# Kernel tuning notes

Hardware: AMD Instinct MI355X
Metric: run time of the kernel (lower is better)

The kernel has to match this reference:

```python
import jax, jax.numpy as jnp
import numpy as np

DEPTH = 256
HEADS = 8
K = 128          # kernel_size == attended axis length (height)
DH = DEPTH // HEADS  # 32
EPS = 1e-5


def _bn(x, gamma, beta, axes):
    # training-mode batch norm (biased variance), per-channel on axis 1
    mean = jnp.mean(x, axis=axes, keepdims=True)
    var = jnp.var(x, axis=axes, keepdims=True)
    shape = [1] * x.ndim
    shape[1] = x.shape[1]
    g = gamma.reshape(shape)
    b = beta.reshape(shape)
    return (x - mean) * jax.lax.rsqrt(var + EPS) * g + b


def setup_inputs() -> dict:
    key = jax.random.key(0)
    ks = jax.random.split(key, 3)
    x = jax.random.normal(ks[0], (2, DEPTH, K, K), dtype=jnp.float32)
    w_kqv = jax.random.normal(ks[1], (2 * DEPTH, DEPTH), dtype=jnp.float32) * 0.05
    rel_encoding = jax.random.normal(ks[2], (2 * DH, 2 * K - 1), dtype=jnp.float32)
    return {
        "x": x,
        "w_kqv": w_kqv,
        "kqv_gamma": jnp.ones((2 * DEPTH,), jnp.float32),
        "kqv_beta": jnp.zeros((2 * DEPTH,), jnp.float32),
        "logits_gamma": jnp.ones((3 * HEADS,), jnp.float32),
        "logits_beta": jnp.zeros((3 * HEADS,), jnp.float32),
        "rel_encoding": rel_encoding,
    }


def reference(x, w_kqv, kqv_gamma, kqv_beta, logits_gamma, logits_beta, rel_encoding):
    B, C, H, W = x.shape  # height_dim=True path
    # (B,C,H,W) -> (B,W,C,H) -> (B*W, C, H)
    xf = jnp.transpose(x, (0, 3, 1, 2)).reshape(B * W, C, H)
    # 1x1 conv == channel matmul
    kqv = jnp.einsum('oc,bch->boh', w_kqv, xf)  # (BW, 2*depth, H)
    kqv = _bn(kqv, kqv_gamma, kqv_beta, axes=(0, 2))
    kqv = kqv.reshape(B * W, HEADS, 2 * DH, H)
    k = kqv[:, :, : DH // 2]            # (BW, h, dh/2, H)
    q = kqv[:, :, DH // 2: DH]          # (BW, h, dh/2, H)
    v = kqv[:, :, DH:]                  # (BW, h, dh,   H)

    # relative position gather: (2*dh, 2K-1) -> (2*dh, K, K)
    idx = (jnp.arange(K)[None, :] - jnp.arange(K)[:, None] + K - 1).reshape(-1)
    rel = rel_encoding[:, idx].reshape(2 * DH, K, K)
    q_enc = rel[: DH // 2]
    k_enc = rel[DH // 2: DH]
    v_enc = rel[DH:]

    qk = jnp.einsum('bhdx,bhdy->bhxy', q, k)
    qr = jnp.einsum('bhdx,dxy->bhxy', q, q_enc)
    kr = jnp.swapaxes(jnp.einsum('bhdx,dxy->bhxy', k, k_enc), 2, 3)
    logits = jnp.concatenate([qk, qr, kr], axis=1)  # (BW, 3*h, K, K)
    logits = _bn(logits, logits_gamma, logits_beta, axes=(0, 2, 3))
    logits = logits.reshape(B * W, 3, HEADS, H, H).sum(axis=1)
    weights = jax.nn.softmax(logits, axis=3)  # (BW, h, K, K)

    attn = jnp.einsum('bhxy,bhdy->bhdx', weights, v)         # (BW, h, dh, H)
    attn_enc = jnp.einsum('bhxy,dxy->bhdx', weights, v_enc)  # (BW, h, dh, H)
    out = (attn + attn_enc).reshape(B, W, DEPTH, H)  # cat+reshape+sum(dim=-2) == add
    out = jnp.transpose(out, (0, 2, 3, 1))  # (B, depth, H, W)
    return out
```

## Files before the change

### kernel.cpp

```cpp
#include <hip/hip_runtime.h>
#include <hip/hip_bf16.h>

#define H 128
#define NB 256
#define OC 512
#define CIN 256
#define NN 16384
#define EPS 1e-5f

#define EQG_OFF 524288
#define EKG_OFF 589824
#define EVG_OFF 655360

typedef __attribute__((ext_vector_type(4))) float f32x4;
typedef __attribute__((ext_vector_type(8))) short bf16x8;
typedef unsigned short u16x8 __attribute__((ext_vector_type(8)));

__device__ __forceinline__ float bf2f(unsigned short u){
    return __uint_as_float(((unsigned int)u) << 16);
}
__device__ __forceinline__ unsigned short f2bf(float f){
    unsigned int r;
    asm("v_cvt_pk_bf16_f32 %0, %1, %2" : "=v"(r) : "v"(f), "v"(f));
    return (unsigned short)r;
}
__device__ __forceinline__ float ldin(const void* p, size_t i, bool f32){
    return f32 ? ((const float*)p)[i] : bf2f(((const unsigned short*)p)[i]);
}
__device__ __forceinline__ short ld_bf16(const void* p, size_t i, bool f32){
    if (f32) return (short)f2bf(((const float*)p)[i]);
    return ((const short*)p)[i];
}
__device__ __forceinline__ bool probe_f32(const void* gamma_ones){
    return *(const unsigned int*)gamma_ones == 0x3F800000u;
}

template<bool F32>
__device__ __forceinline__ void gemm_body(const void* __restrict__ w,
                                          const void* __restrict__ x,
                                          unsigned short* __restrict__ c1,
                                          short (*As)[128][40], short (*Bs)[64][40])
{
    const int m0 = blockIdx.x * 128;
    const int n0 = blockIdx.y * 64;
    const int b0 = blockIdx.z;
    const int t  = threadIdx.x;
    const int lane = t & 63, wv = t >> 6;
    const int wm = wv & 1, wn = wv >> 1;
    const int lm = lane & 15, quad = lane >> 4;
    const size_t xb = (size_t)b0 * CIN * NN;
    const int am = t >> 1, ak = (t & 1) * 16;
    const int bn = t & 63, bk = (t >> 6) * 8;

    float4 pa[4]; float pb[8];
    u16x8 qa[2]; unsigned short qb[8];

    auto load_tile = [&](int k0){
        if constexpr (F32){
            const float* wp = (const float*)w + (size_t)(m0+am)*CIN + k0 + ak;
            #pragma unroll
            for (int q=0;q<4;q++) pa[q] = *(const float4*)(wp + 4*q);
            const float* xp = (const float*)x + xb + (size_t)(k0+bk)*NN + n0 + bn;
            #pragma unroll
            for (int i=0;i<8;i++) pb[i] = xp[(size_t)i*NN];
        } else {
            const unsigned short* wp = (const unsigned short*)w + (size_t)(m0+am)*CIN + k0 + ak;
            qa[0] = *(const u16x8*)wp; qa[1] = *(const u16x8*)(wp+8);
            const unsigned short* xp = (const unsigned short*)x + xb + (size_t)(k0+bk)*NN + n0 + bn;
            #pragma unroll
            for (int i=0;i<8;i++) qb[i] = xp[(size_t)i*NN];
        }
    };
    auto store_tile = [&](int buf){
        if constexpr (F32){
            short ta[16];
            #pragma unroll
            for (int q=0;q<4;q++){
                ta[4*q+0]=(short)f2bf(pa[q].x); ta[4*q+1]=(short)f2bf(pa[q].y);
                ta[4*q+2]=(short)f2bf(pa[q].z); ta[4*q+3]=(short)f2bf(pa[q].w);
            }
            *(bf16x8*)&As[buf][am][ak]   = *(bf16x8*)&ta[0];
            *(bf16x8*)&As[buf][am][ak+8] = *(bf16x8*)&ta[8];
            #pragma unroll
            for (int i=0;i<8;i++) Bs[buf][bn][bk+i] = (short)f2bf(pb[i]);
        } else {
            *(u16x8*)&As[buf][am][ak]   = qa[0];
            *(u16x8*)&As[buf][am][ak+8] = qa[1];
            #pragma unroll
            for (int i=0;i<8;i++) Bs[buf][bn][bk+i] = (short)qb[i];
        }
    };

    f32x4 acc[4][2];
    #pragma unroll
    for (int i=0;i<4;i++){ acc[i][0]=(f32x4){0,0,0,0}; acc[i][1]=(f32x4){0,0,0,0}; }

    load_tile(0); store_tile(0); __syncthreads();
    for (int kk=0; kk<8; ++kk){
        const int cur = kk & 1;
        if (kk < 7) load_tile((kk+1)*32);
        bf16x8 af[4], bfB[2];
        #pragma unroll
        for (int i=0;i<4;i++) af[i]  = *(const bf16x8*)&As[cur][wm*64 + i*16 + lm][quad*8];
        #pragma unroll
        for (int j=0;j<2;j++) bfB[j] = *(const bf16x8*)&Bs[cur][wn*32 + j*16 + lm][quad*8];
        #pragma unroll
        for (int i=0;i<4;i++)
            #pragma unroll
            for (int j=0;j<2;j++)
                acc[i][j] = __builtin_amdgcn_mfma_f32_16x16x32_bf16(af[i], bfB[j], acc[i][j], 0,0,0);
        if (kk < 7) store_tile(cur ^ 1);
        __syncthreads();
    }
    #pragma unroll
    for (int i=0;i<4;i++){
        #pragma unroll
        for (int j=0;j<2;j++){
            int n = n0 + wn*32 + j*16 + lm;
            #pragma unroll
            for (int r=0;r<4;r++){
                int m = m0 + wm*64 + i*16 + quad*4 + r;
                c1[((size_t)b0*OC + m)*NN + n] = f2bf(acc[i][j][r]);
            }
        }
    }
}

__global__ __launch_bounds__(256) void k_gemm(const void* __restrict__ w,
                                              const void* __restrict__ x,
                                              unsigned short* __restrict__ c1,
                                              const void* __restrict__ probe)
{
    __shared__ short As[2][128][40];
    __shared__ short Bs[2][64][40];
    if (probe_f32(probe)) gemm_body<true >(w, x, c1, As, Bs);
    else                  gemm_body<false>(w, x, c1, As, Bs);
}

__global__ __launch_bounds__(256) void k_bn_transpose(const unsigned short* __restrict__ c1,
        unsigned short* __restrict__ kqvt,
        const void* __restrict__ gamma, const void* __restrict__ beta)
{
    __shared__ short T[128][130];
    __shared__ float red[8];
    __shared__ float sc_sh[2];
    const bool f32 = probe_f32(gamma);
    const int o = blockIdx.x;
    const int t = threadIdx.x;
    const int lane = t & 63, wv = t >> 6;
    const u16x8* r08 = (const u16x8*)(c1 + (size_t)o*NN);
    const u16x8* r18 = (const u16x8*)(c1 + ((size_t)OC + o)*NN);
    float s=0.f, ss=0.f;
    #pragma unroll
    for (int i=0;i<8;i++){
        u16x8 a = r08[t + i*256];
        u16x8 b = r18[t + i*256];
        #pragma unroll
        for (int e=0;e<8;e++){
            float va = bf2f(a[e]); s += va; ss = fmaf(va,va,ss);
            float vb = bf2f(b[e]); s += vb; ss = fmaf(vb,vb,ss);
        }
    }
    #pragma unroll
    for (int off=1; off<64; off<<=1){ s += __shfl_xor(s,off); ss += __shfl_xor(ss,off); }
    if (lane==0){ red[wv*2] = s; red[wv*2+1] = ss; }
    __syncthreads();
    if (t==0){
        float st=0.f, sq=0.f;
        for (int i=0;i<4;i++){ st += red[i*2]; sq += red[i*2+1]; }
        float mean = st * (1.f/32768.f);
        float var  = sq * (1.f/32768.f) - mean*mean;
        float scale = ldin(gamma, o, f32) * rsqrtf(var + EPS);
        sc_sh[0] = scale;
        sc_sh[1] = ldin(beta, o, f32) - mean*scale;
    }
    __syncthreads();
    const float scale = sc_sh[0], shift = sc_sh[1];
    for (int b0=0;b0<2;b0++){
        const u16x8* r8 = b0 ? r18 : r08;
        #pragma unroll
        for (int i=0;i<8;i++){
            int vi = t + i*256;
            u16x8 a = r8[vi];
            int n0_ = vi*8;
            int h = n0_ >> 7, ww = n0_ & 127;
            #pragma unroll
            for (int e=0;e<8;e++) T[ww+e][h] = (short)a[e];
        }
        __syncthreads();
        #pragma unroll
        for (int i=0;i<8;i++){
            int vi = t + i*256;
            int ww = vi >> 4, h8 = (vi & 15)*8;
            u16x8 tv = *(const u16x8*)&T[ww][h8];
            unsigned short outv[8];
            #pragma unroll
            for (int e=0;e<8;e++)
                outv[e] = f2bf(fmaf(bf2f((unsigned short)tv[e]), scale, shift));
            *(u16x8*)&kqvt[(((size_t)(b0*128 + ww))*OC + o)*H + h8] = *(u16x8*)outv;
        }
        __syncthreads();
    }
}

__global__ __launch_bounds__(256) void k_encpre(const void* __restrict__ relenc,
        float* __restrict__ ws, const void* __restrict__ probe)
{
    __shared__ float E[16][256];
    const bool f32 = probe_f32(probe);
    const int grp = blockIdx.x;
    const int t = threadIdx.x;
    if (grp == 2){
        unsigned short* ev = (unsigned short*)ws + EVG_OFF;
        for (int i = t; i < 32*264; i += 256){
            int d = i / 264, j = i - d*264;
            ev[i] = (j < 255) ? (unsigned short)ld_bf16(relenc, (size_t)(32+d)*255 + j, f32) : 0;
        }
        return;
    }
    for (int i = t; i < 16*255; i += 256){
        int d = i / 255, j = i - d*255;
        E[d][j] = bf2f((unsigned short)ld_bf16(relenc, (size_t)(grp*16 + d)*255 + j, f32));
    }
    __syncthreads();
    float* Rout = ws + 256  + grp*2048;
    float* Cout = ws + 8192 + grp*32768;
    {
        const int d = t >> 4, e = t & 15;
        const float* Ed = E[d]; const float* Ee = E[e];
        float c = 0.f;
        for (int j = 0; j < 128; ++j) c = fmaf(Ed[j], Ee[j], c);
        float* Cp = Cout + (d*16+e)*128;
        Cp[127] = c;
        for (int xx = 126; xx >= 0; --xx){
            c += Ed[254-xx]*Ee[254-xx] - Ed[126-xx]*Ee[126-xx];
            Cp[xx] = c;
        }
    }
    if (t < 16){
        const float* Ed = E[t];
        float r = 0.f;
        for (int j = 0; j < 128; ++j) r += Ed[j];
        float* Rp = Rout + t*128;
        Rp[127] = r;
        for (int xx = 126; xx >= 0; --xx){
            r += Ed[254-xx] - Ed[126-xx];
            Rp[xx] = r;
        }
    }
}

__global__ __launch_bounds__(256) void k_stats2(const unsigned short* __restrict__ kqvt,
        const float* __restrict__ ws, float* __restrict__ stats)
{
    __shared__ short QK[2][16][128];
    __shared__ float wr[4][6];
    const int b = blockIdx.x >> 3, head = blockIdx.x & 7;
    const int t = threadIdx.x;
    const int lane = t & 63, wv = t >> 6;
    const int lm = lane & 15, quad = lane >> 4;
    const unsigned short* base = kqvt + ((size_t)b*OC + head*64)*H;
    for (int i = t; i < 512; i += 256){
        int arr = i >> 8, d = (i >> 4) & 15, c = i & 15;
        *(u16x8*)&QK[arr][d][c*8] = *(const u16x8*)&base[(size_t)(arr*16 + d)*H + c*8];
    }
    __syncthreads();

    float s_qk = 0.f, q_qk = 0.f;
    if (wv == 0){
        f32x4 gq  = (f32x4){0,0,0,0}, gk  = (f32x4){0,0,0,0};
        f32x4 gq1 = (f32x4){0,0,0,0}, gk1 = (f32x4){0,0,0,0};
        bf16x8 ones;
        #pragma unroll
        for (int i=0;i<8;i++) ones[i] = (short)0x3F80;
        #pragma unroll
        for (int xt=0; xt<4; ++xt){
            bf16x8 fq = *(const bf16x8*)&QK[1][lm][xt*32 + quad*8];
            bf16x8 fk = *(const bf16x8*)&QK[0][lm][xt*32 + quad*8];
            gq  = __builtin_amdgcn_mfma_f32_16x16x32_bf16(fq, fq,   gq,  0,0,0);
            gk  = __builtin_amdgcn_mfma_f32_16x16x32_bf16(fk, fk,   gk,  0,0,0);
            gq1 = __builtin_amdgcn_mfma_f32_16x16x32_bf16(fq, ones, gq1, 0,0,0);
            gk1 = __builtin_amdgcn_mfma_f32_16x16x32_bf16(fk, ones, gk1, 0,0,0);
        }
        #pragma unroll
        for (int r=0;r<4;r++) q_qk += gq[r]*gk[r];
        if (lm == 0){
            #pragma unroll
            for (int r=0;r<4;r++) s_qk += gq1[r]*gk1[r];
        }
    }

    const int half = t >> 7;
    const int x = t & 127;
    float col[16];
    #pragma unroll
    for (int d=0; d<16; ++d) col[d] = bf2f((unsigned short)QK[1-half][d][x]);
    const float* Rp = ws + 256  + half*2048;
    const float* Cp = ws + 8192 + half*32768;
    float sr = 0.f, q2 = 0.f;
    #pragma unroll
    for (int d=0; d<16; ++d) sr = fmaf(col[d], Rp[d*128 + x], sr);
    for (int d=0; d<16; ++d){
        float qd = col[d];
        #pragma unroll
        for (int e=0; e<16; ++e)
            q2 = fmaf(qd*col[e], Cp[(d*16+e)*128 + x], q2);
    }
    float s_qr = half ? 0.f : sr,  q_qr = half ? 0.f : q2;
    float s_kr = half ? sr : 0.f,  q_kr = half ? q2 : 0.f;

    #pragma unroll
    for (int off=1; off<64; off<<=1){
        s_qk += __shfl_xor(s_qk,off); q_qk += __shfl_xor(q_qk,off);
        s_qr += __shfl_xor(s_qr,off); q_qr += __shfl_xor(q_qr,off);
        s_kr += __shfl_xor(s_kr,off); q_kr += __shfl_xor(q_kr,off);
    }
    if (lane==0){ wr[wv][0]=s_qk; wr[wv][1]=s_qr; wr[wv][2]=s_kr;
                  wr[wv][3]=q_qk; wr[wv][4]=q_qr; wr[wv][5]=q_kr; }
    __syncthreads();
    if (t==0){
        float a0=0,a1=0,a2=0,b0_=0,b1=0,b2=0;
        for (int i=0;i<4;i++){ a0+=wr[i][0]; a1+=wr[i][1]; a2+=wr[i][2];
                               b0_+=wr[i][3]; b1+=wr[i][4]; b2+=wr[i][5]; }
        atomicAdd(&stats[head],      a0);
        atomicAdd(&stats[8+head],    a1);
        atomicAdd(&stats[16+head],   a2);
        atomicAdd(&stats[24+head],   b0_);
        atomicAdd(&stats[32+head],   b1);
        atomicAdd(&stats[40+head],   b2);
    }
}

__global__ void k_scales(const float* __restrict__ stats, float* __restrict__ scales,
                         const void* __restrict__ gamma_l, const void* __restrict__ probe)
{
    const bool f32 = probe_f32(probe);
    int t = threadIdx.x;
    if (t < 24){
        const float inv_cnt = 1.f/4194304.f;
        float mean = stats[t]*inv_cnt;
        float var  = stats[24+t]*inv_cnt - mean*mean;
        scales[t] = ldin(gamma_l, t, f32) * rsqrtf(var + EPS);
    }
}

__global__ void k_escale(const void* __restrict__ relenc, const float* __restrict__ scales,
                         unsigned short* __restrict__ etab, const void* __restrict__ probe)
{
    const bool f32 = probe_f32(probe);
    const int head = blockIdx.x;
    const int t = threadIdx.x;
    const float s1 = scales[8+head], s2 = scales[16+head];
    unsigned short* eq = etab + EQG_OFF + head*8192;
    unsigned short* ek = etab + EKG_OFF + head*8192;
    for (int i = t; i < 8192; i += 256){
        int j = i >> 5, c = i & 31;
        unsigned short vq = 0, vk = 0;
        if (c < 16 && j < 255){
            vq = f2bf(s1 * ldin(relenc, (size_t)c*255 + j, f32));
            vk = f2bf(s2 * ldin(relenc, (size_t)(16+c)*255 + j, f32));
        }
        eq[i] = vq; ek[i] = vk;
    }
}

__global__ __launch_bounds__(256) void k_attn(const unsigned short* __restrict__ kqvt,
        const unsigned short* __restrict__ etab,
        const float* __restrict__ scales,
        void* __restrict__ outp,
        const void* __restrict__ probe)
{
    __shared__ short KA[128][24];
    __shared__ short RW[128][134];
    __shared__ alignas(16) short ZED[16];
    const bool f32 = probe_f32(probe);
    const int blk = blockIdx.x;
    const int b = blk >> 3, head = blk & 7;
    const int b0 = b >> 7, w = b & 127;
    const int t = threadIdx.x;
    const int lane = t & 63, wv = t >> 6;
    const int lm = lane & 15, quad = lane >> 4;
    const unsigned short* base = kqvt + ((size_t)b*OC + head*64)*H;
    const float s0 = scales[head];
    const unsigned short* EQg = etab + EQG_OFF + (size_t)head*8192;
    const unsigned short* EKg = etab + EKG_OFF + (size_t)head*8192;
    const unsigned short* EVg = etab + EVG_OFF;

    {
        int dd = t & 15, xg = (t >> 4) * 8;
        u16x8 kv = *(const u16x8*)&base[dd*H + xg];
        #pragma unroll
        for (int e=0;e<8;e++) KA[xg+e][dd] = (short)kv[e];
    }
    bf16x8 aq[2];
    #pragma unroll
    for (int u=0;u<2;u++){
        aq[u] = (bf16x8){0,0,0,0,0,0,0,0};
        if (quad < 2){
            const int x = (2*wv+u)*16 + lm;
            const unsigned short* qp = base + (16+quad*8)*H + x;
            #pragma unroll
            for (int e=0;e<8;e++) aq[u][e] = (short)qp[(size_t)e*H];
        }
    }
    if (t < 16) ZED[t] = 0;
    __syncthreads();

    bf16x8 akk[2];
    #pragma unroll
    for (int u=0;u<2;u++){
        akk[u] = (bf16x8){0,0,0,0,0,0,0,0};
        if (quad < 2) akk[u] = *(const bf16x8*)&KA[(2*wv+u)*16 + lm][quad*8];
    }

    f32x4 qacc[2][8];
    #pragma unroll
    for (int u=0;u<2;u++){
        const int mt = 2*wv + u;
        #pragma unroll
        for (int yt=0; yt<8; ++yt){
            const short* pb = (quad < 2) ? &KA[yt*16 + lm][quad*8] : &ZED[0];
            bf16x8 bk = *(const bf16x8*)pb;
            qacc[u][yt] = __builtin_amdgcn_mfma_f32_16x16x32_bf16(aq[u], bk,
                            (f32x4){0.f,0.f,0.f,0.f}, 0,0,0);
        }
        for (int jt=0; jt<16; ++jt){
            int sdiag = mt + jt;
            if (sdiag < 7 || sdiag > 15) continue;
            bf16x8 bq = *(const bf16x8*)&EQg[(size_t)(jt*16 + lm)*32 + quad*8];
            f32x4 cq = __builtin_amdgcn_mfma_f32_16x16x32_bf16(aq[u], bq,
                         (f32x4){0.f,0.f,0.f,0.f}, 0,0,0);
            int j = jt*16 + lm;
            #pragma unroll
            for (int r=0;r<4;r++){
                int x = mt*16 + quad*4 + r;
                int y = x + j - 127;
                if ((unsigned)y < 128u) RW[x][y] = (short)f2bf(cq[r]);
            }
        }
    }
    __syncthreads();

    #pragma unroll
    for (int u=0;u<2;u++){
        const int mt = 2*wv + u;
        for (int jt=0; jt<16; ++jt){
            int sdiag = mt + jt;
            if (sdiag < 7 || sdiag > 15) continue;
            bf16x8 bkE = *(const bf16x8*)&EKg[(size_t)(jt*16 + lm)*32 + quad*8];
            f32x4 ck = __builtin_amdgcn_mfma_f32_16x16x32_bf16(akk[u], bkE,
                         (f32x4){0.f,0.f,0.f,0.f}, 0,0,0);
            int j = jt*16 + lm;
            #pragma unroll
            for (int r=0;r<4;r++){
                int y = mt*16 + quad*4 + r;
                int x = y + j - 127;
                if ((unsigned)x < 128u){
                    float cur = bf2f((unsigned short)RW[x][y]);
                    RW[x][y] = (short)f2bf(cur + ck[r]);
                }
            }
        }
    }
    __syncthreads();

    #pragma unroll
    for (int u=0;u<2;u++){
        const int mt = 2*wv + u;
        #pragma unroll
        for (int r=0;r<4;r++){
            const int x = mt*16 + quad*4 + r;
            float v[8]; float mx = -1e30f;
            #pragma unroll
            for (int yt=0; yt<8; ++yt){
                v[yt] = fmaf(s0, qacc[u][yt][r], bf2f((unsigned short)RW[x][yt*16 + lm]));
                mx = fmaxf(mx, v[yt]);
            }
            mx = fmaxf(mx, __shfl_xor(mx,1));
            mx = fmaxf(mx, __shfl_xor(mx,2));
            mx = fmaxf(mx, __shfl_xor(mx,4));
            mx = fmaxf(mx, __shfl_xor(mx,8));
            float sum = 0.f;
            #pragma unroll
            for (int yt=0; yt<8; ++yt){ v[yt] = __expf(v[yt]-mx); sum += v[yt]; }
            sum += __shfl_xor(sum,1);
            sum += __shfl_xor(sum,2);
            sum += __shfl_xor(sum,4);
            sum += __shfl_xor(sum,8);
            float inv = 1.f/sum;
            #pragma unroll
            for (int yt=0; yt<8; ++yt)
                RW[x][yt*16 + lm] = (short)f2bf(v[yt]*inv);
        }
    }
    __syncthreads();

    f32x4 o[2][2];
    #pragma unroll
    for (int u=0;u<2;u++){ o[u][0]=(f32x4){0,0,0,0}; o[u][1]=(f32x4){0,0,0,0}; }
    #pragma unroll
    for (int kt=0; kt<4; ++kt){
        bf16x8 bv0 = *(const bf16x8*)&base[(size_t)(32+lm)*H + kt*32 + quad*8];
        bf16x8 bv1 = *(const bf16x8*)&base[(size_t)(48+lm)*H + kt*32 + quad*8];
        #pragma unroll
        for (int u=0;u<2;u++){
            bf16x8 aw = *(const bf16x8*)&RW[(2*wv+u)*16 + lm][kt*32 + quad*8];
            o[u][0] = __builtin_amdgcn_mfma_f32_16x16x32_bf16(aw, bv0, o[u][0], 0,0,0);
            o[u][1] = __builtin_amdgcn_mfma_f32_16x16x32_bf16(aw, bv1, o[u][1], 0,0,0);
        }
    }
    for (int kt=0; kt<8; ++kt){
        bf16x8 be0 = *(const bf16x8*)&EVg[(size_t)lm*264      + kt*32 + quad*8];
        bf16x8 be1 = *(const bf16x8*)&EVg[(size_t)(16+lm)*264 + kt*32 + quad*8];
        #pragma unroll
        for (int u=0;u<2;u++){
            const int mt = 2*wv + u;
            int lo = mt*16 + kt*32 - 127;
            if (lo > 127 || lo + 46 < 0) continue;
            int xg = mt*16 + lm;
            int y0 = xg + kt*32 + quad*8 - 127;
            short g[8];
            #pragma unroll
            for (int jj=0;jj<8;jj++){
                int y = y0 + jj;
                g[jj] = ((unsigned)y < 128u) ? RW[xg][y] : (short)0;
            }
            bf16x8 ag = *(bf16x8*)g;
            o[u][0] = __builtin_amdgcn_mfma_f32_16x16x32_bf16(ag, be0, o[u][0], 0,0,0);
            o[u][1] = __builtin_amdgcn_mfma_f32_16x16x32_bf16(ag, be1, o[u][1], 0,0,0);
        }
    }
    #pragma unroll
    for (int u=0;u<2;u++){
        #pragma unroll
        for (int nt=0; nt<2; ++nt){
            int d = nt*16 + lm;
            size_t cb = ((size_t)(b0*256 + head*32 + d))*16384 + (size_t)w;
            #pragma unroll
            for (int r=0;r<4;r++){
                int x = (2*wv+u)*16 + quad*4 + r;
                if (f32) ((float*)outp)[cb + (size_t)x*128] = o[u][nt][r];
                else ((unsigned short*)outp)[cb + (size_t)x*128] = f2bf(o[u][nt][r]);
            }
        }
    }
}

extern "C" void kernel_launch(void* const* d_in, const int* in_sizes, int n_in,
                              void* d_out, int out_size, void* d_ws, size_t ws_size,
                              hipStream_t stream)
{
    (void)in_sizes; (void)n_in; (void)out_size;
    const void* x      = d_in[0];
    const void* w_kqv  = d_in[1];
    const void* kqv_g  = d_in[2];
    const void* kqv_b  = d_in[3];
    const void* log_g  = d_in[4];
    const void* relenc = d_in[6];

    if (ws_size < (size_t)64*1024*1024) return;
    unsigned short* C1   = (unsigned short*)d_ws;
    unsigned short* KQVT = C1 + 16777216;
    float* WS     = (float*)d_ws;
    float* STATS  = WS;
    float* SCALES = WS + 48;
    unsigned short* ETAB = (unsigned short*)d_ws;

    dim3 g1(OC/128, NN/64, 2);
    k_gemm<<<g1, 256, 0, stream>>>(w_kqv, x, C1, kqv_g);
    k_bn_transpose<<<512, 256, 0, stream>>>(C1, KQVT, kqv_g, kqv_b);
    hipMemsetAsync(STATS, 0, 48*sizeof(float), stream);
    k_encpre<<<3, 256, 0, stream>>>(relenc, WS, kqv_g);
    k_stats2<<<2048, 256, 0, stream>>>(KQVT, WS, STATS);
    k_scales<<<1, 64, 0, stream>>>(STATS, SCALES, log_g, kqv_g);
    k_escale<<<8, 256, 0, stream>>>(relenc, SCALES, ETAB, kqv_g);
    k_attn<<<2048, 256, 0, stream>>>(KQVT, ETAB, SCALES, d_out, kqv_g);
}
```

Before: 370.0 us.

## Enlarge GEMM N-tile, split BN-transpose by batch, and tighten attention loop bounds

The projection GEMM tile grows from 128x64 to 128x128 per block, with vectorized 16-byte LDS stores for the B tile, so each loaded W tile is reused across more columns. The BN-transpose kernel now launches one block per batch instead of looping over both batches, doubling parallelism, though each block still recomputes the full channel statistics. Reductions in the BN and stats kernels use four partial accumulators to shorten dependency chains. The attention kernel's relative-position loops drop their runtime skip checks in favour of fixed-trip unrolled ranges, and the RW LDS row padding shrinks, which may change bank-conflict behaviour.

```diff
diff --git a/kernel.cpp b/kernel.cpp
--- a/kernel.cpp
+++ b/kernel.cpp
@@ -39,10 +39,10 @@
 __device__ __forceinline__ void gemm_body(const void* __restrict__ w,
                                           const void* __restrict__ x,
                                           unsigned short* __restrict__ c1,
-                                          short (*As)[128][40], short (*Bs)[64][40])
+                                          short (*As)[128][40], short (*Bs)[128][40])
 {
     const int m0 = blockIdx.x * 128;
-    const int n0 = blockIdx.y * 64;
+    const int n0 = blockIdx.y * 128;
     const int b0 = blockIdx.z;
     const int t  = threadIdx.x;
     const int lane = t & 63, wv = t >> 6;
@@ -50,10 +50,10 @@
     const int lm = lane & 15, quad = lane >> 4;
     const size_t xb = (size_t)b0 * CIN * NN;
     const int am = t >> 1, ak = (t & 1) * 16;
-    const int bn = t & 63, bk = (t >> 6) * 8;
-
-    float4 pa[4]; float pb[8];
-    u16x8 qa[2]; unsigned short qb[8];
+    const int bn = t & 127, bk = (t >> 7) * 16;
+
+    float4 pa[4]; float pb[16];
+    u16x8 qa[2]; unsigned short qb[16];
 
     auto load_tile = [&](int k0){
         if constexpr (F32){
@@ -62,13 +62,13 @@
             for (int q=0;q<4;q++) pa[q] = *(const float4*)(wp + 4*q);
             const float* xp = (const float*)x + xb + (size_t)(k0+bk)*NN + n0 + bn;
             #pragma unroll
-            for (int i=0;i<8;i++) pb[i] = xp[(size_t)i*NN];
+            for (int i=0;i<16;i++) pb[i] = xp[(size_t)i*NN];
         } else {
             const unsigned short* wp = (const unsigned short*)w + (size_t)(m0+am)*CIN + k0 + ak;
             qa[0] = *(const u16x8*)wp; qa[1] = *(const u16x8*)(wp+8);
             const unsigned short* xp = (const unsigned short*)x + xb + (size_t)(k0+bk)*NN + n0 + bn;
             #pragma unroll
-            for (int i=0;i<8;i++) qb[i] = xp[(size_t)i*NN];
+            for (int i=0;i<16;i++) qb[i] = xp[(size_t)i*NN];
         }
     };
     auto store_tile = [&](int buf){
@@ -81,33 +81,38 @@
             }
             *(bf16x8*)&As[buf][am][ak]   = *(bf16x8*)&ta[0];
             *(bf16x8*)&As[buf][am][ak+8] = *(bf16x8*)&ta[8];
-            #pragma unroll
-            for (int i=0;i<8;i++) Bs[buf][bn][bk+i] = (short)f2bf(pb[i]);
+            short tb[16];
+            #pragma unroll
+            for (int i=0;i<16;i++) tb[i] = (short)f2bf(pb[i]);
+            *(bf16x8*)&Bs[buf][bn][bk]   = *(bf16x8*)&tb[0];
+            *(bf16x8*)&Bs[buf][bn][bk+8] = *(bf16x8*)&tb[8];
         } else {
             *(u16x8*)&As[buf][am][ak]   = qa[0];
             *(u16x8*)&As[buf][am][ak+8] = qa[1];
-            #pragma unroll
-            for (int i=0;i<8;i++) Bs[buf][bn][bk+i] = (short)qb[i];
+            *(u16x8*)&Bs[buf][bn][bk]   = *(u16x8*)&qb[0];
+            *(u16x8*)&Bs[buf][bn][bk+8] = *(u16x8*)&qb[8];
         }
     };
 
-    f32x4 acc[4][2];
-    #pragma unroll
-    for (int i=0;i<4;i++){ acc[i][0]=(f32x4){0,0,0,0}; acc[i][1]=(f32x4){0,0,0,0}; }
+    f32x4 acc[4][4];
+    #pragma unroll
+    for (int i=0;i<4;i++)
+        #pragma unroll
+        for (int j=0;j<4;j++) acc[i][j]=(f32x4){0,0,0,0};
 
     load_tile(0); store_tile(0); __syncthreads();
     for (int kk=0; kk<8; ++kk){
         const int cur = kk & 1;
         if (kk < 7) load_tile((kk+1)*32);
-        bf16x8 af[4], bfB[2];
+        bf16x8 af[4], bfB[4];
         #pragma unroll
         for (int i=0;i<4;i++) af[i]  = *(const bf16x8*)&As[cur][wm*64 + i*16 + lm][quad*8];
         #pragma unroll
-        for (int j=0;j<2;j++) bfB[j] = *(const bf16x8*)&Bs[cur][wn*32 + j*16 + lm][quad*8];
+        for (int j=0;j<4;j++) bfB[j] = *(const bf16x8*)&Bs[cur][wn*64 + j*16 + lm][quad*8];
         #pragma unroll
         for (int i=0;i<4;i++)
             #pragma unroll
-            for (int j=0;j<2;j++)
+            for (int j=0;j<4;j++)
                 acc[i][j] = __builtin_amdgcn_mfma_f32_16x16x32_bf16(af[i], bfB[j], acc[i][j], 0,0,0);
         if (kk < 7) store_tile(cur ^ 1);
         __syncthreads();
@@ -115,8 +120,8 @@
     #pragma unroll
     for (int i=0;i<4;i++){
         #pragma unroll
-        for (int j=0;j<2;j++){
-            int n = n0 + wn*32 + j*16 + lm;
+        for (int j=0;j<4;j++){
+            int n = n0 + wn*64 + j*16 + lm;
             #pragma unroll
             for (int r=0;r<4;r++){
                 int m = m0 + wm*64 + i*16 + quad*4 + r;
@@ -132,7 +137,7 @@
                                               const void* __restrict__ probe)
 {
     __shared__ short As[2][128][40];
-    __shared__ short Bs[2][64][40];
+    __shared__ short Bs[2][128][40];
     if (probe_f32(probe)) gemm_body<true >(w, x, c1, As, Bs);
     else                  gemm_body<false>(w, x, c1, As, Bs);
 }
@@ -145,22 +150,25 @@
     __shared__ float red[8];
     __shared__ float sc_sh[2];
     const bool f32 = probe_f32(gamma);
-    const int o = blockIdx.x;
+    const int o  = blockIdx.x;
+    const int b0 = blockIdx.y;
     const int t = threadIdx.x;
     const int lane = t & 63, wv = t >> 6;
     const u16x8* r08 = (const u16x8*)(c1 + (size_t)o*NN);
     const u16x8* r18 = (const u16x8*)(c1 + ((size_t)OC + o)*NN);
-    float s=0.f, ss=0.f;
+    float sp[4] = {0,0,0,0}, qp[4] = {0,0,0,0};
     #pragma unroll
     for (int i=0;i<8;i++){
         u16x8 a = r08[t + i*256];
         u16x8 b = r18[t + i*256];
         #pragma unroll
         for (int e=0;e<8;e++){
-            float va = bf2f(a[e]); s += va; ss = fmaf(va,va,ss);
-            float vb = bf2f(b[e]); s += vb; ss = fmaf(vb,vb,ss);
-        }
-    }
+            float va = bf2f(a[e]); sp[e&3] += va; qp[e&3] = fmaf(va,va,qp[e&3]);
+            float vb = bf2f(b[e]); sp[e&3] += vb; qp[e&3] = fmaf(vb,vb,qp[e&3]);
+        }
+    }
+    float s = (sp[0]+sp[1])+(sp[2]+sp[3]);
+    float ss = (qp[0]+qp[1])+(qp[2]+qp[3]);
     #pragma unroll
     for (int off=1; off<64; off<<=1){ s += __shfl_xor(s,off); ss += __shfl_xor(ss,off); }
     if (lane==0){ red[wv*2] = s; red[wv*2+1] = ss; }
@@ -176,30 +184,27 @@
     }
     __syncthreads();
     const float scale = sc_sh[0], shift = sc_sh[1];
-    for (int b0=0;b0<2;b0++){
-        const u16x8* r8 = b0 ? r18 : r08;
-        #pragma unroll
-        for (int i=0;i<8;i++){
-            int vi = t + i*256;
-            u16x8 a = r8[vi];
-            int n0_ = vi*8;
-            int h = n0_ >> 7, ww = n0_ & 127;
-            #pragma unroll
-            for (int e=0;e<8;e++) T[ww+e][h] = (short)a[e];
-        }
-        __syncthreads();
-        #pragma unroll
-        for (int i=0;i<8;i++){
-            int vi = t + i*256;
-            int ww = vi >> 4, h8 = (vi & 15)*8;
-            u16x8 tv = *(const u16x8*)&T[ww][h8];
-            unsigned short outv[8];
-            #pragma unroll
-            for (int e=0;e<8;e++)
-                outv[e] = f2bf(fmaf(bf2f((unsigned short)tv[e]), scale, shift));
-            *(u16x8*)&kqvt[(((size_t)(b0*128 + ww))*OC + o)*H + h8] = *(u16x8*)outv;
-        }
-        __syncthreads();
+    const u16x8* r8 = b0 ? r18 : r08;
+    #pragma unroll
+    for (int i=0;i<8;i++){
+        int vi = t + i*256;
+        u16x8 a = r8[vi];
+        int n0_ = vi*8;
+        int h = n0_ >> 7, ww = n0_ & 127;
+        #pragma unroll
+        for (int e=0;e<8;e++) T[ww+e][h] = (short)a[e];
+    }
+    __syncthreads();
+    #pragma unroll
+    for (int i=0;i<8;i++){
+        int vi = t + i*256;
+        int ww = vi >> 4, h8 = (vi & 15)*8;
+        u16x8 tv = *(const u16x8*)&T[ww][h8];
+        unsigned short outv[8];
+        #pragma unroll
+        for (int e=0;e<8;e++)
+            outv[e] = f2bf(fmaf(bf2f((unsigned short)tv[e]), scale, shift));
+        *(u16x8*)&kqvt[(((size_t)(b0*128 + ww))*OC + o)*H + h8] = *(u16x8*)outv;
     }
 }
 
@@ -297,15 +302,17 @@
     for (int d=0; d<16; ++d) col[d] = bf2f((unsigned short)QK[1-half][d][x]);
     const float* Rp = ws + 256  + half*2048;
     const float* Cp = ws + 8192 + half*32768;
-    float sr = 0.f, q2 = 0.f;
+    float sr = 0.f;
     #pragma unroll
     for (int d=0; d<16; ++d) sr = fmaf(col[d], Rp[d*128 + x], sr);
+    float q2p[4] = {0,0,0,0};
     for (int d=0; d<16; ++d){
         float qd = col[d];
         #pragma unroll
         for (int e=0; e<16; ++e)
-            q2 = fmaf(qd*col[e], Cp[(d*16+e)*128 + x], q2);
-    }
+            q2p[e&3] = fmaf(qd*col[e], Cp[(d*16+e)*128 + x], q2p[e&3]);
+    }
+    float q2 = (q2p[0]+q2p[1]) + (q2p[2]+q2p[3]);
     float s_qr = half ? 0.f : sr,  q_qr = half ? 0.f : q2;
     float s_kr = half ? sr : 0.f,  q_kr = half ? q2 : 0.f;
 
@@ -371,7 +378,7 @@
         const void* __restrict__ probe)
 {
     __shared__ short KA[128][24];
-    __shared__ short RW[128][134];
+    __shared__ short RW[128][130];
     __shared__ alignas(16) short ZED[16];
     const bool f32 = probe_f32(probe);
     const int blk = blockIdx.x;
@@ -424,9 +431,9 @@
             qacc[u][yt] = __builtin_amdgcn_mfma_f32_16x16x32_bf16(aq[u], bk,
                             (f32x4){0.f,0.f,0.f,0.f}, 0,0,0);
         }
-        for (int jt=0; jt<16; ++jt){
-            int sdiag = mt + jt;
-            if (sdiag < 7 || sdiag > 15) continue;
+        #pragma unroll
+        for (int jj=0; jj<9; ++jj){
+            const int jt = 7 - mt + jj;
             bf16x8 bq = *(const bf16x8*)&EQg[(size_t)(jt*16 + lm)*32 + quad*8];
             f32x4 cq = __builtin_amdgcn_mfma_f32_16x16x32_bf16(aq[u], bq,
                          (f32x4){0.f,0.f,0.f,0.f}, 0,0,0);
@@ -444,9 +451,9 @@
     #pragma unroll
     for (int u=0;u<2;u++){
         const int mt = 2*wv + u;
-        for (int jt=0; jt<16; ++jt){
-            int sdiag = mt + jt;
-            if (sdiag < 7 || sdiag > 15) continue;
+        #pragma unroll
+        for (int jj=0; jj<9; ++jj){
+            const int jt = 7 - mt + jj;
             bf16x8 bkE = *(const bf16x8*)&EKg[(size_t)(jt*16 + lm)*32 + quad*8];
             f32x4 ck = __builtin_amdgcn_mfma_f32_16x16x32_bf16(akk[u], bkE,
                          (f32x4){0.f,0.f,0.f,0.f}, 0,0,0);
@@ -509,21 +516,22 @@
             o[u][1] = __builtin_amdgcn_mfma_f32_16x16x32_bf16(aw, bv1, o[u][1], 0,0,0);
         }
     }
-    for (int kt=0; kt<8; ++kt){
-        bf16x8 be0 = *(const bf16x8*)&EVg[(size_t)lm*264      + kt*32 + quad*8];
-        bf16x8 be1 = *(const bf16x8*)&EVg[(size_t)(16+lm)*264 + kt*32 + quad*8];
-        #pragma unroll
-        for (int u=0;u<2;u++){
-            const int mt = 2*wv + u;
-            int lo = mt*16 + kt*32 - 127;
-            if (lo > 127 || lo + 46 < 0) continue;
-            int xg = mt*16 + lm;
+    #pragma unroll
+    for (int u=0;u<2;u++){
+        const int mt = 2*wv + u;
+        const int ktlo = (112 - mt*16) >> 5;
+        const int xg = mt*16 + lm;
+        #pragma unroll
+        for (int jj=0; jj<5; ++jj){
+            const int kt = ktlo + jj;
+            bf16x8 be0 = *(const bf16x8*)&EVg[(size_t)lm*264      + kt*32 + quad*8];
+            bf16x8 be1 = *(const bf16x8*)&EVg[(size_t)(16+lm)*264 + kt*32 + quad*8];
             int y0 = xg + kt*32 + quad*8 - 127;
             short g[8];
             #pragma unroll
-            for (int jj=0;jj<8;jj++){
-                int y = y0 + jj;
-                g[jj] = ((unsigned)y < 128u) ? RW[xg][y] : (short)0;
+            for (int jjj=0;jjj<8;jjj++){
+                int y = y0 + jjj;
+                g[jjj] = ((unsigned)y < 128u) ? RW[xg][y] : (short)0;
             }
             bf16x8 ag = *(bf16x8*)g;
             o[u][0] = __builtin_amdgcn_mfma_f32_16x16x32_bf16(ag, be0, o[u][0], 0,0,0);
@@ -566,9 +574,9 @@
     float* SCALES = WS + 48;
     unsigned short* ETAB = (unsigned short*)d_ws;
 
-    dim3 g1(OC/128, NN/64, 2);
+    dim3 g1(OC/128, NN/128, 2);
     k_gemm<<<g1, 256, 0, stream>>>(w_kqv, x, C1, kqv_g);
-    k_bn_transpose<<<512, 256, 0, stream>>>(C1, KQVT, kqv_g, kqv_b);
+    k_bn_transpose<<<dim3(512,2), 256, 0, stream>>>(C1, KQVT, kqv_g, kqv_b);
     hipMemsetAsync(STATS, 0, 48*sizeof(float), stream);
     k_encpre<<<3, 256, 0, stream>>>(relenc, WS, kqv_g);
     k_stats2<<<2048, 256, 0, stream>>>(KQVT, WS, STATS);
```

Result: faster. 345.0 us (-6.8%).
